# Optimization experiments

Hardware: AMD Instinct MI355X
Metric: run time of the kernel (lower is better)

The kernel has to match this reference:

```python
import jax, jax.numpy as jnp
import numpy as np

B, C, Ci = 4, 256, 128
T, H, W = 16, 28, 28
EPS = 1e-5  # BatchNorm eps


def conv1x1(x, w, b):
    # 1x1x1 Conv3d == channel-mixing GEMM. x: (b,c,t,h,w), w: (o,c), b: (o,)
    return jnp.einsum('bcthw,oc->bothw', x, w) + b[None, :, None, None, None]


def pool2(x):
    # MaxPool3d(kernel_size=2, stride=2); all spatial dims are even here.
    b, c, t, h, w = x.shape
    return x.reshape(b, c, t // 2, 2, h // 2, 2, w // 2, 2).max(axis=(3, 5, 7))


def setup_inputs() -> dict:
    key = jax.random.key(0)
    ks = jax.random.split(key, 9)
    kaiming_in = (2.0 / C) ** 0.5   # kaiming_normal_ fan_in for 1x1 conv
    kaiming_mid = (2.0 / Ci) ** 0.5
    return {
        'x': jax.random.normal(ks[0], (B, C, T, H, W), jnp.float32),
        'w_g': jax.random.normal(ks[1], (Ci, C), jnp.float32) * kaiming_in,
        'b_g': jnp.zeros((Ci,), jnp.float32),
        'w_theta': jax.random.normal(ks[2], (Ci, C), jnp.float32) * kaiming_in,
        'b_theta': jnp.zeros((Ci,), jnp.float32),
        'w_phi': jax.random.normal(ks[3], (Ci, C), jnp.float32) * kaiming_in,
        'b_phi': jnp.zeros((Ci,), jnp.float32),
        'w_W': jax.random.normal(ks[4], (C, Ci), jnp.float32) * kaiming_mid,
        'b_W': jnp.zeros((C,), jnp.float32),
        'bn_gamma': 1.0 + 0.1 * jax.random.normal(ks[5], (C,), jnp.float32),
        'bn_beta': 0.1 * jax.random.normal(ks[6], (C,), jnp.float32),
        'bn_mean': 0.1 * jax.random.normal(ks[7], (C,), jnp.float32),
        'bn_var': jax.random.uniform(ks[8], (C,), jnp.float32, 0.5, 1.5),
    }


def reference(x, w_g, b_g, w_theta, b_theta, w_phi, b_phi, w_W, b_W,
              bn_gamma, bn_beta, bn_mean, bn_var):
    b = x.shape[0]
    # g/phi are sub-sampled (MaxPool3d(2)) -> M = N/8 keys
    g_x = pool2(conv1x1(x, w_g, b_g)).reshape(b, Ci, -1).transpose(0, 2, 1)    # (b, M, Ci)
    theta_x = conv1x1(x, w_theta, b_theta).reshape(b, Ci, -1).transpose(0, 2, 1)  # (b, N, Ci)
    phi_x = pool2(conv1x1(x, w_phi, b_phi)).reshape(b, Ci, -1)                # (b, Ci, M)
    f = jnp.einsum('bnc,bcm->bnm', theta_x, phi_x)                            # (b, N, M)
    attn = jax.nn.softmax(f, axis=-1)
    y = jnp.einsum('bnm,bmc->bnc', attn, g_x)                                 # (b, N, Ci)
    y = y.transpose(0, 2, 1).reshape(b, Ci, T, H, W)
    W_y = conv1x1(y, w_W, b_W)
    # BatchNorm3d (eval mode with running stats)
    scale = (bn_gamma / jnp.sqrt(bn_var + EPS))[None, :, None, None, None]
    W_y = (W_y - bn_mean[None, :, None, None, None]) * scale + bn_beta[None, :, None, None, None]
    return W_y + x
```

## Files before the change

### kernel.cpp

```cpp
#include <hip/hip_runtime.h>
#include <math.h>

typedef _Float16 f16;
typedef _Float16 f16x8 __attribute__((ext_vector_type(8)));
typedef float f32x4 __attribute__((ext_vector_type(4)));
typedef float f32x16 __attribute__((ext_vector_type(16)));

#define BB 4
#define CC 256
#define CI 128
#define NN 12544
#define MM 1568
#define TP 8
#define HP 14
#define WP 14

#define OFF_W3T 0u
#define OFF_WWH 196608u
#define OFF_B3  262144u
#define OFF_SC  263168u
#define OFF_OFB 264192u
#define OFF_XT  265216u
#define OFF_TPG (OFF_XT + 25690112u)
#define OFF_PHI (OFF_TPG + 38535168u)
#define OFF_G   (OFF_PHI + 1605632u)
#define OFF_Y   (OFF_G + 1605632u)
#define WS_NEED (OFF_Y + 12845056u)

static __device__ __forceinline__ f32x4 mfma16(f16x8 a, f16x8 b, f32x4 c) {
    return __builtin_amdgcn_mfma_f32_16x16x32_f16(a, b, c, 0, 0, 0);
}
static __device__ __forceinline__ f32x16 mfma32(f16x8 a, f16x8 b, f32x16 c) {
    return __builtin_amdgcn_mfma_f32_32x32x16_f16(a, b, c, 0, 0, 0);
}
static __device__ __forceinline__ unsigned pkrtz(float a, float b) {
    auto h = __builtin_amdgcn_cvt_pkrtz(a, b);
    return __builtin_bit_cast(unsigned, h);
}

__global__ __launch_bounds__(256) void k_prep(
    const float* __restrict__ wg, const float* __restrict__ bg,
    const float* __restrict__ wth, const float* __restrict__ bth_,
    const float* __restrict__ wph, const float* __restrict__ bph,
    const float* __restrict__ wW, const float* __restrict__ bW,
    const float* __restrict__ gam, const float* __restrict__ bet,
    const float* __restrict__ mean, const float* __restrict__ var,
    f16* __restrict__ w3t, f16* __restrict__ wWh, f16* __restrict__ b3,
    float* __restrict__ sc, float* __restrict__ ofb) {
    int r = blockIdx.x;
    int c = threadIdx.x;
    const float* src = (r < 128) ? (wth + (size_t)r * CC)
                     : (r < 256) ? (wph + (size_t)(r - 128) * CC)
                                 : (wg + (size_t)(r - 256) * CC);
    w3t[(size_t)r * CC + c] = (f16)src[c];
    if (c == 0) {
        float bv = (r < 128) ? bth_[r] : (r < 256) ? bph[r - 128] : bg[r - 256];
        b3[r] = (f16)bv;
    }
    if (r < 256) {
        if (c < 128) wWh[(size_t)r * CI + c] = (f16)wW[(size_t)r * CI + c];
        if (c == 0) {
            float s = gam[r] * rsqrtf(var[r] + 1e-5f);
            sc[r] = s;
            ofb[r] = (bW[r] - mean[r]) * s + bet[r];
        }
    }
}

__global__ __launch_bounds__(256) void k_xt(const float* __restrict__ x, f16* __restrict__ xT) {
    int bid = blockIdx.x;
    int b = bid / (196 * 4); int rem = bid % (196 * 4);
    int nt = rem / 4, ct = rem % 4;
    int n0 = nt * 64, c0 = ct * 64;
    __shared__ float tile[64][65];
    const float* xb = x + (size_t)b * CC * NN;
    for (int p = 0; p < 16; ++p) {
        int idx = p * 256 + threadIdx.x;
        int i = idx >> 6, j = idx & 63;
        tile[i][j] = xb[(size_t)(c0 + i) * NN + n0 + j];
    }
    __syncthreads();
    f16* xTb = xT + (size_t)b * NN * CC;
    for (int p = 0; p < 16; ++p) {
        int idx = p * 256 + threadIdx.x;
        int n = idx >> 6, c = idx & 63;
        xTb[(size_t)(n0 + n) * CC + c0 + c] = (f16)tile[c][n];
    }
}

__global__ __launch_bounds__(256) void k_conv(const f16* __restrict__ xT, const f16* __restrict__ w3t,
                                              const f16* __restrict__ b3, f16* __restrict__ tpg) {
    int bid = blockIdx.x;
    int b = bid / (98 * 3); int rem = bid % (98 * 3);
    int nt = rem / 3, ct = rem % 3;
    int n0 = nt * 128, co0 = ct * 128;
    __shared__ f16 As[128 * 64];
    __shared__ f16 Bs[128 * 64];
    const f16* xb = xT + (size_t)b * NN * CC + (size_t)n0 * CC;
    const f16* wb = w3t + (size_t)co0 * CC;
    int wv = threadIdx.x >> 6, ln = threadIdx.x & 63;
    int wr = (wv & 1) * 64, wc = (wv >> 1) * 64;
    f32x4 acc[4][4];
    for (int i = 0; i < 4; ++i) for (int j = 0; j < 4; ++j)
        for (int r = 0; r < 4; ++r) acc[i][j][r] = 0.f;
    for (int ks = 0; ks < 4; ++ks) {
        for (int s = threadIdx.x; s < 1024; s += 256) {
            int row = s >> 3, sl = s & 7;
            f16x8 va = *(const f16x8*)(xb + (size_t)row * CC + ks * 64 + sl * 8);
            *(f16x8*)(As + row * 64 + ((sl * 8) ^ ((row & 7) << 3))) = va;
            f16x8 vb = *(const f16x8*)(wb + (size_t)row * CC + ks * 64 + sl * 8);
            *(f16x8*)(Bs + row * 64 + ((sl * 8) ^ ((row & 7) << 3))) = vb;
        }
        __syncthreads();
        for (int kc = 0; kc < 2; ++kc) {
            int klo = kc * 32 + ((ln >> 4) * 8);
            f16x8 af[4], bf[4];
            for (int i = 0; i < 4; ++i) {
                int rn = wr + i * 16 + (ln & 15);
                af[i] = *(const f16x8*)(As + rn * 64 + (klo ^ ((rn & 7) << 3)));
                int rc = wc + i * 16 + (ln & 15);
                bf[i] = *(const f16x8*)(Bs + rc * 64 + (klo ^ ((rc & 7) << 3)));
            }
            for (int i = 0; i < 4; ++i)
                for (int j = 0; j < 4; ++j)
                    acc[i][j] = mfma16(af[i], bf[j], acc[i][j]);
        }
        __syncthreads();
    }
    f16* ob = tpg + (size_t)b * NN * 384 + (size_t)n0 * 384 + co0;
    for (int j = 0; j < 4; ++j) {
        float bias = (float)b3[co0 + wc + j * 16 + (ln & 15)];
        for (int i = 0; i < 4; ++i)
            for (int r = 0; r < 4; ++r) {
                int n = wr + i * 16 + (ln >> 4) * 4 + r;
                int co = wc + j * 16 + (ln & 15);
                ob[(size_t)n * 384 + co] = (f16)(acc[i][j][r] + bias);
            }
    }
}

__global__ __launch_bounds__(256) void k_pool(const f16* __restrict__ tpg,
                                              f16* __restrict__ phi, f16* __restrict__ gx) {
    int bid = blockIdx.x;
    int b = bid / (TP * HP); int rem = bid % (TP * HP);
    int tp = rem / HP, hp = rem % HP;
    const f16* base = tpg + (size_t)b * NN * 384;
    for (int idx = threadIdx.x; idx < WP * 128; idx += 256) {
        int wp = idx >> 7, ci = idx & 127;
        f16 mp = (f16)(-60000.0f), mg = (f16)(-60000.0f);
        for (int dt = 0; dt < 2; ++dt)
            for (int dh = 0; dh < 2; ++dh)
                for (int dw = 0; dw < 2; ++dw) {
                    int n = (2 * tp + dt) * 784 + (2 * hp + dh) * 28 + (2 * wp + dw);
                    f16 vp = base[(size_t)n * 384 + 128 + ci];
                    f16 vg = base[(size_t)n * 384 + 256 + ci];
                    mp = vp > mp ? vp : mp;
                    mg = vg > mg ? vg : mg;
                }
        int m = tp * 196 + hp * 14 + wp;
        phi[(size_t)b * MM * CI + (size_t)m * CI + ci] = mp;
        gx[(size_t)b * CI * MM + (size_t)ci * MM + m] = mg;
    }
}


template<int S>
__device__ __forceinline__ void stage_load(const f16* __restrict__ phib, const f16* __restrict__ gb,
                                           int m0, int tid, f16x8* sp, f16x8* sg) {
    #pragma unroll
    for (int p = 0; p < S / 16; ++p) {
        int s = p * 256 + tid;
        int row = s >> 4, sl = s & 15;
        sp[p] = *(const f16x8*)(phib + (size_t)(m0 + row) * CI + sl * 8);
    }
    #pragma unroll
    for (int p = 0; p < S / 16; ++p) {
        int s = p * 256 + tid;
        int row = (S == 64) ? (s >> 3) : (s >> 2);
        int sl  = (S == 64) ? (s & 7) : (s & 3);
        sg[p] = *(const f16x8*)(gb + (size_t)row * MM + m0 + sl * 8);
    }
}

template<int S>
__device__ __forceinline__ void stage_write(f16* __restrict__ Bp, f16* __restrict__ Bg,
                                            int tid, const f16x8* sp, const f16x8* sg) {
    #pragma unroll
    for (int p = 0; p < S / 16; ++p) {
        int s = p * 256 + tid;
        int row = s >> 4, sl = s & 15;
        *(f16x8*)(Bp + row * 128 + ((sl * 8) ^ ((row & 15) << 3))) = sp[p];
    }
    #pragma unroll
    for (int p = 0; p < S / 16; ++p) {
        int s = p * 256 + tid;
        int row = (S == 64) ? (s >> 3) : (s >> 2);
        int sl  = (S == 64) ? (s & 7) : (s & 3);
        *(f16x8*)(Bg + row * 64 + ((sl * 8) ^ ((row & 7) << 3))) = sg[p];
    }
}

template<int KF>
__device__ __forceinline__ void attn_chunk(const f16* __restrict__ Bp, const f16* __restrict__ Bg,
                                           const f16x8* bth, f32x16* yv,
                                           float& mrun, float& lrun, int lq, int hi) {
    f32x16 qk[KF];
    __builtin_amdgcn_s_setprio(1);
    #pragma unroll
    for (int kf = 0; kf < KF; ++kf) {
        #pragma unroll
        for (int r = 0; r < 16; ++r) qk[kf][r] = 0.f;
        int row = kf * 32 + lq;
        const f16* rp = Bp + row * 128;
        int sw = (row & 15) << 3;
        #pragma unroll
        for (int ks = 0; ks < 8; ++ks)
            qk[kf] = mfma32(*(const f16x8*)(rp + ((ks * 16 + hi * 8) ^ sw)), bth[ks], qk[kf]);
    }
    __builtin_amdgcn_s_setprio(0);
    float t[8];
    #pragma unroll
    for (int i = 0; i < 8; ++i) {
        t[i] = fmaxf(qk[0][i], qk[0][i + 8]);
        if (KF == 2) t[i] = fmaxf(t[i], fmaxf(qk[KF - 1][i], qk[KF - 1][i + 8]));
    }
    #pragma unroll
    for (int s = 4; s >= 1; s >>= 1)
        #pragma unroll
        for (int i = 0; i < s; ++i) t[i] = fmaxf(t[i], t[i + s]);
    float mx = fmaxf(t[0], __shfl_xor(t[0], 32));
    if (__any(mx > mrun + 8.f)) {
        float mnew = fmaxf(mrun, mx);
        float scl = __expf(mrun - mnew);
        lrun *= scl;
        #pragma unroll
        for (int c = 0; c < 4; ++c)
            #pragma unroll
            for (int r = 0; r < 16; ++r) yv[c][r] *= scl;
        mrun = mnew;
    }
    float ps = 0.f;
    #pragma unroll
    for (int kf = 0; kf < KF; ++kf)
        #pragma unroll
        for (int r = 0; r < 16; ++r) {
            float p = __expf(qk[kf][r] - mrun);
            qk[kf][r] = p;
            ps += p;
        }
    ps += __shfl_xor(ps, 32);
    lrun += ps;
    #pragma unroll
    for (int s = 0; s < 2 * KF; ++s) {
        const int kf = s >> 1;
        const int base = (s & 1) * 8;
        unsigned A0 = pkrtz(qk[kf][base + 0], qk[kf][base + 1]);
        unsigned A1 = pkrtz(qk[kf][base + 2], qk[kf][base + 3]);
        unsigned B0 = pkrtz(qk[kf][base + 4], qk[kf][base + 5]);
        unsigned B1 = pkrtz(qk[kf][base + 6], qk[kf][base + 7]);
        unsigned g0 = (unsigned)__shfl_xor((int)(hi ? A0 : B0), 32);
        unsigned g1 = (unsigned)__shfl_xor((int)(hi ? A1 : B1), 32);
        union { unsigned u[4]; f16x8 v; } fr;
        fr.u[0] = hi ? g0 : A0;
        fr.u[1] = hi ? g1 : A1;
        fr.u[2] = hi ? B0 : g0;
        fr.u[3] = hi ? B1 : g1;
        __builtin_amdgcn_s_setprio(1);
        #pragma unroll
        for (int c = 0; c < 4; ++c) {
            int row = c * 32 + lq;
            f16x8 gfr = *(const f16x8*)(Bg + row * 64 + ((s * 16 + hi * 8) ^ ((row & 7) << 3)));
            yv[c] = mfma32(gfr, fr.v, yv[c]);
        }
        __builtin_amdgcn_s_setprio(0);
    }
}

__global__ __launch_bounds__(256, 2) void k_attn(const f16* __restrict__ tpg, const f16* __restrict__ phi,
                                                 const f16* __restrict__ gx, f16* __restrict__ y) {
    int bid = blockIdx.x;
    int b = bid / 98; int nt = bid % 98;
    int n0 = nt * 128;
    __shared__ f16 Bp[64 * 128];
    __shared__ f16 Bg[128 * 64];
    int tid = threadIdx.x;
    int wv = tid >> 6, ln = tid & 63, hi = ln >> 5, lq = ln & 31;
    f16x8 bth[8];
    {
        const f16* rowp = tpg + ((size_t)b * NN + n0 + wv * 32 + lq) * 384;
        #pragma unroll
        for (int ks = 0; ks < 8; ++ks)
            bth[ks] = *(const f16x8*)(rowp + ks * 16 + hi * 8);
    }
    f32x16 yv[4];
    #pragma unroll
    for (int c = 0; c < 4; ++c)
        #pragma unroll
        for (int r = 0; r < 16; ++r) yv[c][r] = 0.f;
    float mrun = -1e30f, lrun = 0.f;
    const f16* phib = phi + (size_t)b * MM * CI;
    const f16* gb = gx + (size_t)b * CI * MM;

    f16x8 sp[4], sg[4];
    stage_load<64>(phib, gb, 0, tid, sp, sg);
    stage_write<64>(Bp, Bg, tid, sp, sg);
    __syncthreads();
    for (int t = 0; t < 23; ++t) {
        stage_load<64>(phib, gb, (t + 1) * 64, tid, sp, sg);
        attn_chunk<2>(Bp, Bg, bth, yv, mrun, lrun, lq, hi);
        __syncthreads();
        stage_write<64>(Bp, Bg, tid, sp, sg);
        __syncthreads();
    }
    stage_load<32>(phib, gb, 1536, tid, sp, sg);
    attn_chunk<2>(Bp, Bg, bth, yv, mrun, lrun, lq, hi);
    __syncthreads();
    stage_write<32>(Bp, Bg, tid, sp, sg);
    __syncthreads();
    attn_chunk<1>(Bp, Bg, bth, yv, mrun, lrun, lq, hi);

    float inv = 1.f / lrun;
    f16* yb = y + ((size_t)b * NN + n0 + wv * 32 + lq) * CI;
    #pragma unroll
    for (int c = 0; c < 4; ++c)
        #pragma unroll
        for (int k = 0; k < 4; ++k) {
            int ci = c * 32 + k * 8 + hi * 4;
            uint2 st;
            st.x = pkrtz(yv[c][4 * k + 0] * inv, yv[c][4 * k + 1] * inv);
            st.y = pkrtz(yv[c][4 * k + 2] * inv, yv[c][4 * k + 3] * inv);
            *(uint2*)(yb + ci) = st;
        }
}

__global__ __launch_bounds__(256) void k_out(const f16* __restrict__ wWh, const f16* __restrict__ y,
                                             const float* __restrict__ x, const float* __restrict__ sc,
                                             const float* __restrict__ ofb, float* __restrict__ out) {
    int bid = blockIdx.x;
    int b = bid / (196 * 2); int rem = bid % (196 * 2);
    int nt = rem >> 1, ct = rem & 1;
    int n0 = nt * 64, co0 = ct * 128;
    __shared__ f16 Ws[128 * 128];
    __shared__ f16 Ys[64 * 128];
    for (int s = threadIdx.x; s < 128 * 16; s += 256) {
        int row = s >> 4, sl = s & 15;
        f16x8 v = *(const f16x8*)(wWh + (size_t)(co0 + row) * CI + sl * 8);
        *(f16x8*)(Ws + row * 128 + ((sl * 8) ^ ((row & 7) << 3))) = v;
    }
    const f16* yb = y + (size_t)b * NN * CI + (size_t)n0 * CI;
    for (int s = threadIdx.x; s < 64 * 16; s += 256) {
        int row = s >> 4, sl = s & 15;
        f16x8 v = *(const f16x8*)(yb + (size_t)row * CI + sl * 8);
        *(f16x8*)(Ys + row * 128 + ((sl * 8) ^ ((row & 7) << 3))) = v;
    }
    __syncthreads();
    int wv = threadIdx.x >> 6, ln = threadIdx.x & 63;
    int wc = (wv >> 1) * 64, wn = (wv & 1) * 32;
    f32x4 acc[4][2];
    for (int i = 0; i < 4; ++i) for (int j = 0; j < 2; ++j)
        for (int r = 0; r < 4; ++r) acc[i][j][r] = 0.f;
    for (int kc = 0; kc < 4; ++kc) {
        int klo = kc * 32 + (ln >> 4) * 8;
        f16x8 afr[4], bfr[2];
        for (int i = 0; i < 4; ++i) {
            int rc = wc + i * 16 + (ln & 15);
            afr[i] = *(const f16x8*)(Ws + rc * 128 + (klo ^ ((rc & 7) << 3)));
        }
        for (int j = 0; j < 2; ++j) {
            int rn = wn + j * 16 + (ln & 15);
            bfr[j] = *(const f16x8*)(Ys + rn * 128 + (klo ^ ((rn & 7) << 3)));
        }
        for (int i = 0; i < 4; ++i)
            for (int j = 0; j < 2; ++j)
                acc[i][j] = mfma16(afr[i], bfr[j], acc[i][j]);
    }
    const float* xb = x + (size_t)b * CC * NN;
    float* ob = out + (size_t)b * CC * NN;
    for (int i = 0; i < 4; ++i)
        for (int j = 0; j < 2; ++j)
            for (int r = 0; r < 4; ++r) {
                int co = co0 + wc + i * 16 + (ln >> 4) * 4 + r;
                int n = n0 + wn + j * 16 + (ln & 15);
                size_t idx = (size_t)co * NN + n;
                ob[idx] = acc[i][j][r] * sc[co] + ofb[co] + xb[idx];
            }
}

extern "C" void kernel_launch(void* const* d_in, const int* in_sizes, int n_in,
                              void* d_out, int out_size, void* d_ws, size_t ws_size,
                              hipStream_t stream) {
    const float* x    = (const float*)d_in[0];
    const float* wg   = (const float*)d_in[1];
    const float* bg   = (const float*)d_in[2];
    const float* wth  = (const float*)d_in[3];
    const float* bth  = (const float*)d_in[4];
    const float* wph  = (const float*)d_in[5];
    const float* bph  = (const float*)d_in[6];
    const float* wW   = (const float*)d_in[7];
    const float* bW   = (const float*)d_in[8];
    const float* gam  = (const float*)d_in[9];
    const float* bet  = (const float*)d_in[10];
    const float* mean = (const float*)d_in[11];
    const float* var  = (const float*)d_in[12];
    if (ws_size < (size_t)WS_NEED) return;
    char* ws = (char*)d_ws;
    f16* w3t = (f16*)(ws + OFF_W3T);
    f16* wWh = (f16*)(ws + OFF_WWH);
    f16* b3  = (f16*)(ws + OFF_B3);
    float* sc  = (float*)(ws + OFF_SC);
    float* ofb = (float*)(ws + OFF_OFB);
    f16* xT  = (f16*)(ws + OFF_XT);
    f16* tpg = (f16*)(ws + OFF_TPG);
    f16* phi = (f16*)(ws + OFF_PHI);
    f16* gx  = (f16*)(ws + OFF_G);
    f16* yy  = (f16*)(ws + OFF_Y);
    float* out = (float*)d_out;

    k_prep<<<dim3(384), dim3(256), 0, stream>>>(wg, bg, wth, bth, wph, bph, wW, bW,
                                                gam, bet, mean, var, w3t, wWh, b3, sc, ofb);
    k_xt  <<<dim3(BB * 196 * 4), dim3(256), 0, stream>>>(x, xT);
    k_conv<<<dim3(BB * 98 * 3), dim3(256), 0, stream>>>(xT, w3t, b3, tpg);
    k_pool<<<dim3(BB * TP * HP), dim3(256), 0, stream>>>(tpg, phi, gx);
    k_attn<<<dim3(BB * 98), dim3(256), 0, stream>>>(tpg, phi, gx, yy);
    k_out <<<dim3(BB * 196 * 2), dim3(256), 0, stream>>>(wWh, yy, x, sc, ofb, out);
}
```

Baseline: 146.4 us.

## Use direct global-to-LDS loads with double buffering in conv and attention kernels

Replaces the register-staged global→LDS tile loads in k_conv and k_attn with global_load_lds DMA-style loads into double-buffered shared memory. The swizzle moves to the source address, so the next tile is fetched while the current one is consumed and one barrier per iteration is removed. Shared memory per block grows (64KB in both kernels), which may lower occupancy, and the handling of the tail chunk in attention is rewritten.

Measured after the change: 148.4 us. About the same (+1.3%).

```diff
diff --git a/kernel.cpp b/kernel.cpp
--- a/kernel.cpp
+++ b/kernel.cpp
@@ -36,6 +36,10 @@
 static __device__ __forceinline__ unsigned pkrtz(float a, float b) {
     auto h = __builtin_amdgcn_cvt_pkrtz(a, b);
     return __builtin_bit_cast(unsigned, h);
+}
+static __device__ __forceinline__ void gload16(const f16* g, f16* l) {
+    __builtin_amdgcn_global_load_lds((const __attribute__((address_space(1))) void*)g,
+                                     (__attribute__((address_space(3))) void*)l, 16, 0, 0);
 }
 
 __global__ __launch_bounds__(256) void k_prep(
@@ -94,43 +98,70 @@
     int b = bid / (98 * 3); int rem = bid % (98 * 3);
     int nt = rem / 3, ct = rem % 3;
     int n0 = nt * 128, co0 = ct * 128;
-    __shared__ f16 As[128 * 64];
-    __shared__ f16 Bs[128 * 64];
+    __shared__ f16 SB[2][16384];
     const f16* xb = xT + (size_t)b * NN * CC + (size_t)n0 * CC;
     const f16* wb = w3t + (size_t)co0 * CC;
-    int wv = threadIdx.x >> 6, ln = threadIdx.x & 63;
+    int tid = threadIdx.x;
+    int wv = tid >> 6, ln = tid & 63;
     int wr = (wv & 1) * 64, wc = (wv >> 1) * 64;
+    int k0 = wv * 4;
+    const f16* sA[4]; const f16* sB_[4]; int dA[4], dB[4];
+    #pragma unroll
+    for (int i = 0; i < 4; ++i) {
+        int s16 = (k0 + i) * 64 + ln;
+        int row = s16 >> 3, sl = s16 & 7;
+        sA[i] = xb + (size_t)row * CC + ((sl ^ (row & 7)) << 3);
+        sB_[i] = wb + (size_t)row * CC + ((sl ^ (row & 7)) << 3);
+        dA[i] = (k0 + i) * 512;
+        dB[i] = 8192 + (k0 + i) * 512;
+    }
     f32x4 acc[4][4];
-    for (int i = 0; i < 4; ++i) for (int j = 0; j < 4; ++j)
-        for (int r = 0; r < 4; ++r) acc[i][j][r] = 0.f;
+    #pragma unroll
+    for (int i = 0; i < 4; ++i)
+        #pragma unroll
+        for (int j = 0; j < 4; ++j)
+            #pragma unroll
+            for (int r = 0; r < 4; ++r) acc[i][j][r] = 0.f;
+    #pragma unroll
+    for (int i = 0; i < 4; ++i) { gload16(sA[i], SB[0] + dA[i]); gload16(sB_[i], SB[0] + dB[i]); }
+    __syncthreads();
     for (int ks = 0; ks < 4; ++ks) {
-        for (int s = threadIdx.x; s < 1024; s += 256) {
-            int row = s >> 3, sl = s & 7;
-            f16x8 va = *(const f16x8*)(xb + (size_t)row * CC + ks * 64 + sl * 8);
-            *(f16x8*)(As + row * 64 + ((sl * 8) ^ ((row & 7) << 3))) = va;
-            f16x8 vb = *(const f16x8*)(wb + (size_t)row * CC + ks * 64 + sl * 8);
-            *(f16x8*)(Bs + row * 64 + ((sl * 8) ^ ((row & 7) << 3))) = vb;
-        }
-        __syncthreads();
+        if (ks < 3) {
+            f16* nb = SB[(ks + 1) & 1];
+            #pragma unroll
+            for (int i = 0; i < 4; ++i) {
+                gload16(sA[i] + (ks + 1) * 64, nb + dA[i]);
+                gload16(sB_[i] + (ks + 1) * 64, nb + dB[i]);
+            }
+        }
+        const f16* As = SB[ks & 1];
+        const f16* Bs = As + 8192;
+        #pragma unroll
         for (int kc = 0; kc < 2; ++kc) {
             int klo = kc * 32 + ((ln >> 4) * 8);
             f16x8 af[4], bf[4];
+            #pragma unroll
             for (int i = 0; i < 4; ++i) {
                 int rn = wr + i * 16 + (ln & 15);
                 af[i] = *(const f16x8*)(As + rn * 64 + (klo ^ ((rn & 7) << 3)));
                 int rc = wc + i * 16 + (ln & 15);
                 bf[i] = *(const f16x8*)(Bs + rc * 64 + (klo ^ ((rc & 7) << 3)));
             }
+            #pragma unroll
             for (int i = 0; i < 4; ++i)
+                #pragma unroll
                 for (int j = 0; j < 4; ++j)
                     acc[i][j] = mfma16(af[i], bf[j], acc[i][j]);
         }
         __syncthreads();
     }
     f16* ob = tpg + (size_t)b * NN * 384 + (size_t)n0 * 384 + co0;
+    #pragma unroll
     for (int j = 0; j < 4; ++j) {
         float bias = (float)b3[co0 + wc + j * 16 + (ln & 15)];
+        #pragma unroll
         for (int i = 0; i < 4; ++i)
+            #pragma unroll
             for (int r = 0; r < 4; ++r) {
                 int n = wr + i * 16 + (ln >> 4) * 4 + r;
                 int co = wc + j * 16 + (ln & 15);
@@ -164,42 +195,6 @@
 }
 
 
-template<int S>
-__device__ __forceinline__ void stage_load(const f16* __restrict__ phib, const f16* __restrict__ gb,
-                                           int m0, int tid, f16x8* sp, f16x8* sg) {
-    #pragma unroll
-    for (int p = 0; p < S / 16; ++p) {
-        int s = p * 256 + tid;
-        int row = s >> 4, sl = s & 15;
-        sp[p] = *(const f16x8*)(phib + (size_t)(m0 + row) * CI + sl * 8);
-    }
-    #pragma unroll
-    for (int p = 0; p < S / 16; ++p) {
-        int s = p * 256 + tid;
-        int row = (S == 64) ? (s >> 3) : (s >> 2);
-        int sl  = (S == 64) ? (s & 7) : (s & 3);
-        sg[p] = *(const f16x8*)(gb + (size_t)row * MM + m0 + sl * 8);
-    }
-}
-
-template<int S>
-__device__ __forceinline__ void stage_write(f16* __restrict__ Bp, f16* __restrict__ Bg,
-                                            int tid, const f16x8* sp, const f16x8* sg) {
-    #pragma unroll
-    for (int p = 0; p < S / 16; ++p) {
-        int s = p * 256 + tid;
-        int row = s >> 4, sl = s & 15;
-        *(f16x8*)(Bp + row * 128 + ((sl * 8) ^ ((row & 15) << 3))) = sp[p];
-    }
-    #pragma unroll
-    for (int p = 0; p < S / 16; ++p) {
-        int s = p * 256 + tid;
-        int row = (S == 64) ? (s >> 3) : (s >> 2);
-        int sl  = (S == 64) ? (s & 7) : (s & 3);
-        *(f16x8*)(Bg + row * 64 + ((sl * 8) ^ ((row & 7) << 3))) = sg[p];
-    }
-}
-
 template<int KF>
 __device__ __forceinline__ void attn_chunk(const f16* __restrict__ Bp, const f16* __restrict__ Bg,
                                            const f16x8* bth, f32x16* yv,
@@ -281,8 +276,7 @@
     int bid = blockIdx.x;
     int b = bid / 98; int nt = bid % 98;
     int n0 = nt * 128;
-    __shared__ f16 Bp[64 * 128];
-    __shared__ f16 Bg[128 * 64];
+    __shared__ f16 SB[2][16384];
     int tid = threadIdx.x;
     int wv = tid >> 6, ln = tid & 63, hi = ln >> 5, lq = ln & 31;
     f16x8 bth[8];
@@ -300,24 +294,44 @@
     float mrun = -1e30f, lrun = 0.f;
     const f16* phib = phi + (size_t)b * MM * CI;
     const f16* gb = gx + (size_t)b * CI * MM;
-
-    f16x8 sp[4], sg[4];
-    stage_load<64>(phib, gb, 0, tid, sp, sg);
-    stage_write<64>(Bp, Bg, tid, sp, sg);
+    int k0 = wv * 4;
+    const f16* sP[4]; const f16* sG[4]; int dP[4], dG[4];
+    #pragma unroll
+    for (int i = 0; i < 4; ++i) {
+        int s16 = (k0 + i) * 64 + ln;
+        int row = s16 >> 4, sl = s16 & 15;
+        sP[i] = phib + (size_t)row * CI + ((sl ^ (row & 15)) << 3);
+        dP[i] = (k0 + i) * 512;
+        int row2 = s16 >> 3, sl2 = s16 & 7;
+        sG[i] = gb + (size_t)row2 * MM + ((sl2 ^ (row2 & 7)) << 3);
+        dG[i] = 8192 + (k0 + i) * 512;
+    }
+    #pragma unroll
+    for (int i = 0; i < 4; ++i) { gload16(sP[i], SB[0] + dP[i]); gload16(sG[i], SB[0] + dG[i]); }
     __syncthreads();
-    for (int t = 0; t < 23; ++t) {
-        stage_load<64>(phib, gb, (t + 1) * 64, tid, sp, sg);
-        attn_chunk<2>(Bp, Bg, bth, yv, mrun, lrun, lq, hi);
+    for (int t = 0; t < 24; ++t) {
+        f16* nb = SB[(t + 1) & 1];
+        if (t < 23) {
+            #pragma unroll
+            for (int i = 0; i < 4; ++i) {
+                gload16(sP[i] + (size_t)(t + 1) * 64 * CI, nb + dP[i]);
+                gload16(sG[i] + (size_t)(t + 1) * 64, nb + dG[i]);
+            }
+        } else {
+            #pragma unroll
+            for (int i = 0; i < 4; ++i) {
+                int s16 = (k0 + i) * 64 + ln;
+                int row = s16 >> 4, sl = s16 & 15;
+                gload16(phib + (size_t)(1536 + (row & 31)) * CI + ((sl ^ (row & 15)) << 3), nb + dP[i]);
+                int row2 = s16 >> 3, sl2 = s16 & 7;
+                gload16(gb + (size_t)row2 * MM + 1536 + (((sl2 ^ (row2 & 7)) & 3) << 3), nb + dG[i]);
+            }
+        }
+        const f16* cb = SB[t & 1];
+        attn_chunk<2>(cb, cb + 8192, bth, yv, mrun, lrun, lq, hi);
         __syncthreads();
-        stage_write<64>(Bp, Bg, tid, sp, sg);
-        __syncthreads();
-    }
-    stage_load<32>(phib, gb, 1536, tid, sp, sg);
-    attn_chunk<2>(Bp, Bg, bth, yv, mrun, lrun, lq, hi);
-    __syncthreads();
-    stage_write<32>(Bp, Bg, tid, sp, sg);
-    __syncthreads();
-    attn_chunk<1>(Bp, Bg, bth, yv, mrun, lrun, lq, hi);
+    }
+    attn_chunk<1>(SB[0], SB[0] + 8192, bth, yv, mrun, lrun, lq, hi);
 
     float inv = 1.f / lrun;
     f16* yb = y + ((size_t)b * NN + n0 + wv * 32 + lq) * CI;
```

## Split attention keys across two wave groups per block and merge softmax partials

Applied to the files above, without the earlier changes.

k_attn now launches 512 threads: two groups of four waves each process half of the key range for the same 128 query rows with separate LDS buffers. Partial max/sum statistics and outputs are combined via LDS using online-softmax rescaling, and group 0 writes the final result. This doubles the waves available to hide latency on an under-filled grid, at the cost of extra LDS, a merge phase, and tighter register limits from the new launch bounds.

After: 350.8 us. 140% more time.

```diff
diff --git a/kernel.cpp b/kernel.cpp
--- a/kernel.cpp
+++ b/kernel.cpp
@@ -276,18 +276,21 @@
     }
 }
 
-__global__ __launch_bounds__(256, 2) void k_attn(const f16* __restrict__ tpg, const f16* __restrict__ phi,
+__global__ __launch_bounds__(512, 4) void k_attn(const f16* __restrict__ tpg, const f16* __restrict__ phi,
                                                  const f16* __restrict__ gx, f16* __restrict__ y) {
     int bid = blockIdx.x;
     int b = bid / 98; int nt = bid % 98;
     int n0 = nt * 128;
-    __shared__ f16 Bp[64 * 128];
-    __shared__ f16 Bg[128 * 64];
+    __shared__ f16 SB[2][16384];
     int tid = threadIdx.x;
     int wv = tid >> 6, ln = tid & 63, hi = ln >> 5, lq = ln & 31;
+    int qw = wv & 3, grp = wv >> 2;
+    int gtid = tid & 255;
+    f16* Bp = &SB[grp][0];
+    f16* Bg = &SB[grp][8192];
     f16x8 bth[8];
     {
-        const f16* rowp = tpg + ((size_t)b * NN + n0 + wv * 32 + lq) * 384;
+        const f16* rowp = tpg + ((size_t)b * NN + n0 + qw * 32 + lq) * 384;
         #pragma unroll
         for (int ks = 0; ks < 8; ++ks)
             bth[ks] = *(const f16x8*)(rowp + ks * 16 + hi * 8);
@@ -300,37 +303,73 @@
     float mrun = -1e30f, lrun = 0.f;
     const f16* phib = phi + (size_t)b * MM * CI;
     const f16* gb = gx + (size_t)b * CI * MM;
+    const int mbase = grp * 768;
 
     f16x8 sp[4], sg[4];
-    stage_load<64>(phib, gb, 0, tid, sp, sg);
-    stage_write<64>(Bp, Bg, tid, sp, sg);
-    __syncthreads();
-    for (int t = 0; t < 23; ++t) {
-        stage_load<64>(phib, gb, (t + 1) * 64, tid, sp, sg);
+    stage_load<64>(phib, gb, mbase, gtid, sp, sg);
+    stage_write<64>(Bp, Bg, gtid, sp, sg);
+    __syncthreads();
+    for (int t = 0; t < 12; ++t) {
+        if (t < 11) stage_load<64>(phib, gb, mbase + (t + 1) * 64, gtid, sp, sg);
+        else if (grp == 0) stage_load<32>(phib, gb, 1536, gtid, sp, sg);
         attn_chunk<2>(Bp, Bg, bth, yv, mrun, lrun, lq, hi);
         __syncthreads();
-        stage_write<64>(Bp, Bg, tid, sp, sg);
+        if (t < 11) stage_write<64>(Bp, Bg, gtid, sp, sg);
+        else if (grp == 0) stage_write<32>(Bp, Bg, gtid, sp, sg);
         __syncthreads();
     }
-    stage_load<32>(phib, gb, 1536, tid, sp, sg);
-    attn_chunk<2>(Bp, Bg, bth, yv, mrun, lrun, lq, hi);
-    __syncthreads();
-    stage_write<32>(Bp, Bg, tid, sp, sg);
-    __syncthreads();
-    attn_chunk<1>(Bp, Bg, bth, yv, mrun, lrun, lq, hi);
-
-    float inv = 1.f / lrun;
-    f16* yb = y + ((size_t)b * NN + n0 + wv * 32 + lq) * CI;
+    if (grp == 0) attn_chunk<1>(Bp, Bg, bth, yv, mrun, lrun, lq, hi);
+    __syncthreads();
+
+    float* Lml = (float*)&SB[0][0];
+    Lml[(wv * 64 + ln) * 2] = mrun;
+    Lml[(wv * 64 + ln) * 2 + 1] = lrun;
+    __syncthreads();
+    float mo = Lml[((wv ^ 4) * 64 + ln) * 2];
+    float lo = Lml[((wv ^ 4) * 64 + ln) * 2 + 1];
+    float M = fmaxf(mrun, mo);
+    float aw = __expf(mrun - M);
+    float L = lrun * aw + lo * __expf(mo - M);
+    float w = aw / L;
     #pragma unroll
     for (int c = 0; c < 4; ++c)
         #pragma unroll
-        for (int k = 0; k < 4; ++k) {
-            int ci = c * 32 + k * 8 + hi * 4;
-            uint2 st;
-            st.x = pkrtz(yv[c][4 * k + 0] * inv, yv[c][4 * k + 1] * inv);
-            st.y = pkrtz(yv[c][4 * k + 2] * inv, yv[c][4 * k + 3] * inv);
-            *(uint2*)(yb + ci) = st;
-        }
+        for (int r = 0; r < 16; ++r) yv[c][r] *= w;
+    f16* sv = &SB[0][0] + 2048;
+    int srow = qw * 64 + ln;
+    if (grp) {
+        #pragma unroll
+        for (int f = 0; f < 8; ++f) {
+            int c = f >> 1, kh = f & 1;
+            union { unsigned u[4]; f16x8 v; } fr;
+            fr.u[0] = pkrtz(yv[c][kh * 8 + 0], yv[c][kh * 8 + 1]);
+            fr.u[1] = pkrtz(yv[c][kh * 8 + 2], yv[c][kh * 8 + 3]);
+            fr.u[2] = pkrtz(yv[c][kh * 8 + 4], yv[c][kh * 8 + 5]);
+            fr.u[3] = pkrtz(yv[c][kh * 8 + 6], yv[c][kh * 8 + 7]);
+            *(f16x8*)(sv + srow * 64 + ((f * 8) ^ ((srow & 7) << 3))) = fr.v;
+        }
+    }
+    __syncthreads();
+    if (!grp) {
+        #pragma unroll
+        for (int f = 0; f < 8; ++f) {
+            int c = f >> 1, kh = f & 1;
+            f16x8 o = *(const f16x8*)(sv + srow * 64 + ((f * 8) ^ ((srow & 7) << 3)));
+            #pragma unroll
+            for (int j = 0; j < 8; ++j) yv[c][kh * 8 + j] += (float)o[j];
+        }
+        f16* yb = y + ((size_t)b * NN + n0 + qw * 32 + lq) * CI;
+        #pragma unroll
+        for (int c = 0; c < 4; ++c)
+            #pragma unroll
+            for (int k = 0; k < 4; ++k) {
+                int ci = c * 32 + k * 8 + hi * 4;
+                uint2 st;
+                st.x = pkrtz(yv[c][4 * k + 0], yv[c][4 * k + 1]);
+                st.y = pkrtz(yv[c][4 * k + 2], yv[c][4 * k + 3]);
+                *(uint2*)(yb + ci) = st;
+            }
+    }
 }
 
 __global__ __launch_bounds__(256) void k_out(const f16* __restrict__ wWh, const f16* __restrict__ y,
@@ -421,6 +460,6 @@
     k_xt  <<<dim3(BB * 196 * 4), dim3(256), 0, stream>>>(x, xT);
     k_conv<<<dim3(BB * 98 * 3), dim3(256), 0, stream>>>(xT, w3t, b3, tpg);
     k_pool<<<dim3(BB * TP * HP), dim3(256), 0, stream>>>(tpg, phi, gx);
-    k_attn<<<dim3(BB * 98), dim3(256), 0, stream>>>(tpg, phi, gx, yy);
+    k_attn<<<dim3(BB * 98), dim3(512), 0, stream>>>(tpg, phi, gx, yy);
     k_out <<<dim3(BB * 196 * 2), dim3(256), 0, stream>>>(wWh, yy, x, sc, ofb, out);
 }
```

## Split attention over keys in two halves and merge partials in output GEMM

Applied to the files above, without the earlier changes.

The attention kernel now splits the 1568 keys into two halves handled by separate blocks, doubling the grid from 392 to 784 blocks. Each half writes a normalized partial output plus its running max and sum, and the output projection kernel merges the two partials with log-sum-exp weights while staging Y into shared memory. The aim is to fill the 256 CUs better, since 392 blocks underuse the MI355X. The cost is an extra partial Y buffer (reusing the xT workspace), extra global traffic, and the theta rows being loaded twice.

Measured after the change: 156.1 us. 6.6% more time.

```diff
diff --git a/kernel.cpp b/kernel.cpp
--- a/kernel.cpp
+++ b/kernel.cpp
@@ -26,6 +26,8 @@
 #define OFF_G   (OFF_PHI + 1605632u)
 #define OFF_Y   (OFF_G + 1605632u)
 #define WS_NEED (OFF_Y + 12845056u)
+#define OFF_Y1  OFF_XT
+#define OFF_ML  (OFF_XT + 12845056u)
 
 static __device__ __forceinline__ f32x4 mfma16(f16x8 a, f16x8 b, f32x4 c) {
     return __builtin_amdgcn_mfma_f32_16x16x32_f16(a, b, c, 0, 0, 0);
@@ -277,17 +279,20 @@
 }
 
 __global__ __launch_bounds__(256, 2) void k_attn(const f16* __restrict__ tpg, const f16* __restrict__ phi,
-                                                 const f16* __restrict__ gx, f16* __restrict__ y) {
+                                                 const f16* __restrict__ gx, f16* __restrict__ y0,
+                                                 f16* __restrict__ y1, float2* __restrict__ ml) {
     int bid = blockIdx.x;
-    int b = bid / 98; int nt = bid % 98;
+    int b = bid / 196; int rem = bid % 196;
+    int nt = rem >> 1, kk = rem & 1;
     int n0 = nt * 128;
     __shared__ f16 Bp[64 * 128];
     __shared__ f16 Bg[128 * 64];
     int tid = threadIdx.x;
     int wv = tid >> 6, ln = tid & 63, hi = ln >> 5, lq = ln & 31;
+    int n = n0 + wv * 32 + lq;
     f16x8 bth[8];
     {
-        const f16* rowp = tpg + ((size_t)b * NN + n0 + wv * 32 + lq) * 384;
+        const f16* rowp = tpg + ((size_t)b * NN + n) * 384;
         #pragma unroll
         for (int ks = 0; ks < 8; ++ks)
             bth[ks] = *(const f16x8*)(rowp + ks * 16 + hi * 8);
@@ -300,27 +305,25 @@
     float mrun = -1e30f, lrun = 0.f;
     const f16* phib = phi + (size_t)b * MM * CI;
     const f16* gb = gx + (size_t)b * CI * MM;
+    const int mbase = kk * 768;
 
     f16x8 sp[4], sg[4];
-    stage_load<64>(phib, gb, 0, tid, sp, sg);
+    stage_load<64>(phib, gb, mbase, tid, sp, sg);
     stage_write<64>(Bp, Bg, tid, sp, sg);
     __syncthreads();
-    for (int t = 0; t < 23; ++t) {
-        stage_load<64>(phib, gb, (t + 1) * 64, tid, sp, sg);
+    for (int t = 0; t < 12; ++t) {
+        if (t < 11) stage_load<64>(phib, gb, mbase + (t + 1) * 64, tid, sp, sg);
+        else if (kk == 0) stage_load<32>(phib, gb, 1536, tid, sp, sg);
         attn_chunk<2>(Bp, Bg, bth, yv, mrun, lrun, lq, hi);
         __syncthreads();
-        stage_write<64>(Bp, Bg, tid, sp, sg);
+        if (t < 11) stage_write<64>(Bp, Bg, tid, sp, sg);
+        else if (kk == 0) stage_write<32>(Bp, Bg, tid, sp, sg);
         __syncthreads();
     }
-    stage_load<32>(phib, gb, 1536, tid, sp, sg);
-    attn_chunk<2>(Bp, Bg, bth, yv, mrun, lrun, lq, hi);
-    __syncthreads();
-    stage_write<32>(Bp, Bg, tid, sp, sg);
-    __syncthreads();
-    attn_chunk<1>(Bp, Bg, bth, yv, mrun, lrun, lq, hi);
+    if (kk == 0) attn_chunk<1>(Bp, Bg, bth, yv, mrun, lrun, lq, hi);
 
     float inv = 1.f / lrun;
-    f16* yb = y + ((size_t)b * NN + n0 + wv * 32 + lq) * CI;
+    f16* yb = (kk ? y1 : y0) + ((size_t)b * NN + n) * CI;
     #pragma unroll
     for (int c = 0; c < 4; ++c)
         #pragma unroll
@@ -331,9 +334,14 @@
             st.y = pkrtz(yv[c][4 * k + 2] * inv, yv[c][4 * k + 3] * inv);
             *(uint2*)(yb + ci) = st;
         }
-}
-
-__global__ __launch_bounds__(256) void k_out(const f16* __restrict__ wWh, const f16* __restrict__ y,
+    if (hi == 0) {
+        float2 v; v.x = mrun; v.y = lrun;
+        ml[((size_t)b * 2 + kk) * NN + n] = v;
+    }
+}
+
+__global__ __launch_bounds__(256) void k_out(const f16* __restrict__ wWh, const f16* __restrict__ y0,
+                                             const f16* __restrict__ y1, const float2* __restrict__ ml,
                                              const float* __restrict__ x, const float* __restrict__ sc,
                                              const float* __restrict__ ofb, float* __restrict__ out) {
     int bid = blockIdx.x;
@@ -347,11 +355,26 @@
         f16x8 v = *(const f16x8*)(wWh + (size_t)(co0 + row) * CI + sl * 8);
         *(f16x8*)(Ws + row * 128 + ((sl * 8) ^ ((row & 7) << 3))) = v;
     }
-    const f16* yb = y + (size_t)b * NN * CI + (size_t)n0 * CI;
+    const size_t ybase = (size_t)b * NN * CI + (size_t)n0 * CI;
+    const float2* mlb = ml + (size_t)b * 2 * NN;
     for (int s = threadIdx.x; s < 64 * 16; s += 256) {
         int row = s >> 4, sl = s & 15;
-        f16x8 v = *(const f16x8*)(yb + (size_t)row * CI + sl * 8);
-        *(f16x8*)(Ys + row * 128 + ((sl * 8) ^ ((row & 7) << 3))) = v;
+        int n = n0 + row;
+        float2 m0 = mlb[n];
+        float2 m1 = mlb[NN + n];
+        float M = fmaxf(m0.x, m1.x);
+        float e0 = __expf(m0.x - M) * m0.y;
+        float e1 = __expf(m1.x - M) * m1.y;
+        float iL = 1.f / (e0 + e1);
+        float w0 = e0 * iL, w1 = e1 * iL;
+        f16x8 v0 = *(const f16x8*)(y0 + ybase + (size_t)row * CI + sl * 8);
+        f16x8 v1 = *(const f16x8*)(y1 + ybase + (size_t)row * CI + sl * 8);
+        union { unsigned u[4]; f16x8 v; } o;
+        #pragma unroll
+        for (int j = 0; j < 4; ++j)
+            o.u[j] = pkrtz(w0 * (float)v0[2 * j] + w1 * (float)v1[2 * j],
+                           w0 * (float)v0[2 * j + 1] + w1 * (float)v1[2 * j + 1]);
+        *(f16x8*)(Ys + row * 128 + ((sl * 8) ^ ((row & 7) << 3))) = o.v;
     }
     __syncthreads();
     int wv = threadIdx.x >> 6, ln = threadIdx.x & 63;
@@ -413,7 +436,9 @@
     f16* tpg = (f16*)(ws + OFF_TPG);
     f16* phi = (f16*)(ws + OFF_PHI);
     f16* gx  = (f16*)(ws + OFF_G);
-    f16* yy  = (f16*)(ws + OFF_Y);
+    f16* yy0 = (f16*)(ws + OFF_Y);
+    f16* yy1 = (f16*)(ws + OFF_Y1);
+    float2* ml = (float2*)(ws + OFF_ML);
     float* out = (float*)d_out;
 
     k_prep<<<dim3(384), dim3(256), 0, stream>>>(wg, bg, wth, bth, wph, bph, wW, bW,
@@ -421,6 +446,6 @@
     k_xt  <<<dim3(BB * 196 * 4), dim3(256), 0, stream>>>(x, xT);
     k_conv<<<dim3(BB * 98 * 3), dim3(256), 0, stream>>>(xT, w3t, b3, tpg);
     k_pool<<<dim3(BB * TP * HP), dim3(256), 0, stream>>>(tpg, phi, gx);
-    k_attn<<<dim3(BB * 98), dim3(256), 0, stream>>>(tpg, phi, gx, yy);
-    k_out <<<dim3(BB * 196 * 2), dim3(256), 0, stream>>>(wWh, yy, x, sc, ofb, out);
-}
+    k_attn<<<dim3(BB * 196), dim3(256), 0, stream>>>(tpg, phi, gx, yy0, yy1, ml);
+    k_out <<<dim3(BB * 196 * 2), dim3(256), 0, stream>>>(wWh, yy0, yy1, ml, x, sc, ofb, out);
+}
```
